# Performance work log

Hardware: AMD Instinct MI355X
Metric: run time of the kernel (lower is better)

The kernel has to match this reference:

```python
import jax, jax.numpy as jnp
import numpy as np


def setup_inputs() -> dict:
    key = jax.random.key(0)
    k1, k2, k3, k4 = jax.random.split(key, 4)
    B, S, E, H = 8, 2048, 1024, 64
    x = jax.random.normal(k1, (B, S, E), dtype=jnp.float32)
    # nn.Linear(E, H, bias=False) weight is (H, E); we store transposed (E, H)
    scale = 1.0 / np.sqrt(E)
    Wk = jax.random.normal(k2, (E, H), dtype=jnp.float32) * scale
    Wq = jax.random.normal(k3, (E, H), dtype=jnp.float32) * scale
    Wv = jax.random.normal(k4, (E, H), dtype=jnp.float32) * scale
    return {"x": x, "Wk": Wk, "Wq": Wq, "Wv": Wv}


def reference(x, Wk, Wq, Wv):
    # x: (B, S, E); projections: (B, S, H)
    k = x @ Wk
    q = x @ Wq
    v = x @ Wv
    H = k.shape[-1]
    # scores: (B, S, S) with 1/sqrt(H) scaling as in the torch code
    scores = jnp.einsum("bqh,bkh->bqk", q, k) * (H ** -0.5)
    S = x.shape[1]
    causal = jnp.triu(jnp.full((S, S), -jnp.inf, dtype=scores.dtype), k=1)
    wei = jax.nn.softmax(scores + causal, axis=-1)
    # dropout p=0.0 -> identity
    return jnp.einsum("bqk,bkh->bqh", wei, v)
```

## Files before the change

kernel.cpp:

```cpp
#include <hip/hip_runtime.h>
#include <hip/hip_bf16.h>

typedef unsigned short ushort_t;
typedef __attribute__((ext_vector_type(8))) short short8;
typedef __attribute__((ext_vector_type(4))) short short4v;
typedef __attribute__((ext_vector_type(4))) float f32x4;

__device__ __forceinline__ float bf2f(ushort_t u) {
    unsigned int x = ((unsigned int)u) << 16;
    float f; __builtin_memcpy(&f, &x, 4); return f;
}
__device__ __forceinline__ ushort_t f2bf(float f) {
    __hip_bfloat16 h = __float2bfloat16(f);
    ushort_t u; __builtin_memcpy(&u, &h, 2); return u;
}
__device__ __forceinline__ unsigned packbf2(float a, float b) {
    return (unsigned)f2bf(a) | ((unsigned)f2bf(b) << 16);
}

constexpr int E  = 1024;
constexpr int Hd = 64;
constexpr int S  = 2048;
constexpr int ROWS = 8 * 2048;
constexpr int NTOT = 192;
constexpr int LST  = 88;

__global__ __launch_bounds__(256)
void prep_wt(const float* __restrict__ Wk, const float* __restrict__ Wq,
             const float* __restrict__ Wv, ushort_t* __restrict__ WT)
{
    int idx = blockIdx.x * 256 + threadIdx.x;
    int n = idx >> 10;
    int kk = idx & 1023;
    const float* W = (n < 64) ? Wq : ((n < 128) ? Wk : Wv);
    int h = n & 63;
    WT[idx] = f2bf(W[kk * Hd + h]);
}

__global__ __launch_bounds__(256)
void proj_v7(const float* __restrict__ x, const ushort_t* __restrict__ WT,
             ushort_t* __restrict__ qo, ushort_t* __restrict__ ko,
             ushort_t* __restrict__ vTo)
{
    __shared__ alignas(16) ushort_t XS[32][LST];

    const int t    = threadIdx.x;
    const int w    = t >> 6;
    const int lane = t & 63;
    const int m    = lane & 15;
    const int g    = lane >> 4;
    const int rb   = blockIdx.x * 32;

    f32x4 accq[2], acck[2], accv[2];
    #pragma unroll
    for (int j = 0; j < 2; ++j) {
        accq[j] = (f32x4){0.f, 0.f, 0.f, 0.f};
        acck[j] = (f32x4){0.f, 0.f, 0.f, 0.f};
        accv[j] = (f32x4){0.f, 0.f, 0.f, 0.f};
    }

    const float* xptr = x + (size_t)(rb + (t >> 3)) * E + (t & 7) * 8;
    const ushort_t* wqp = WT + (size_t)(w * 16 + m) * E + g * 8;
    const ushort_t* wkp = wqp + (size_t)64 * E;
    const ushort_t* wvp = wqp + (size_t)128 * E;

    float4 xp0, xp1;
    short8 pbq[2], pbk[2], pbv[2], cbq[2], cbk[2], cbv[2];

    xp0 = *(const float4*)xptr;
    xp1 = *(const float4*)(xptr + 4);
    #pragma unroll
    for (int kt = 0; kt < 2; ++kt) {
        pbq[kt] = *(const short8*)(wqp + kt * 32);
        pbk[kt] = *(const short8*)(wkp + kt * 32);
        pbv[kt] = *(const short8*)(wvp + kt * 32);
    }

    #pragma unroll 1
    for (int c = 0; c < 16; ++c) {
        {
            uint4 sv;
            sv.x = packbf2(xp0.x, xp0.y);
            sv.y = packbf2(xp0.z, xp0.w);
            sv.z = packbf2(xp1.x, xp1.y);
            sv.w = packbf2(xp1.z, xp1.w);
            *(uint4*)&XS[t >> 3][(t & 7) * 8] = sv;
        }
        #pragma unroll
        for (int kt = 0; kt < 2; ++kt) {
            cbq[kt] = pbq[kt]; cbk[kt] = pbk[kt]; cbv[kt] = pbv[kt];
        }
        __syncthreads();

        if (c < 15) {
            const int k0 = (c + 1) * 64;
            xp0 = *(const float4*)(xptr + k0);
            xp1 = *(const float4*)(xptr + k0 + 4);
            #pragma unroll
            for (int kt = 0; kt < 2; ++kt) {
                pbq[kt] = *(const short8*)(wqp + k0 + kt * 32);
                pbk[kt] = *(const short8*)(wkp + k0 + kt * 32);
                pbv[kt] = *(const short8*)(wvp + k0 + kt * 32);
            }
        }

        #pragma unroll
        for (int kt = 0; kt < 2; ++kt) {
            short8 a0 = *(const short8*)&XS[m][kt * 32 + g * 8];
            short8 a1 = *(const short8*)&XS[16 + m][kt * 32 + g * 8];
            accq[0] = __builtin_amdgcn_mfma_f32_16x16x32_bf16(a0, cbq[kt], accq[0], 0, 0, 0);
            accq[1] = __builtin_amdgcn_mfma_f32_16x16x32_bf16(a1, cbq[kt], accq[1], 0, 0, 0);
            acck[0] = __builtin_amdgcn_mfma_f32_16x16x32_bf16(a0, cbk[kt], acck[0], 0, 0, 0);
            acck[1] = __builtin_amdgcn_mfma_f32_16x16x32_bf16(a1, cbk[kt], acck[1], 0, 0, 0);
            accv[0] = __builtin_amdgcn_mfma_f32_16x16x32_bf16(cbv[kt], a0, accv[0], 0, 0, 0);
            accv[1] = __builtin_amdgcn_mfma_f32_16x16x32_bf16(cbv[kt], a1, accv[1], 0, 0, 0);
        }
        __syncthreads();
    }

    const int col   = w * 16 + m;
    const int batch = rb >> 11;
    const int seq0  = rb & (S - 1);
    #pragma unroll
    for (int mt = 0; mt < 2; ++mt) {
        const int orow = rb + mt * 16 + g * 4;
        #pragma unroll
        for (int r = 0; r < 4; ++r) {
            qo[(size_t)(orow + r) * Hd + col] = f2bf(accq[mt][r] * 0.125f);
            ko[(size_t)(orow + r) * Hd + col] = f2bf(acck[mt][r]);
        }
    }
    #pragma unroll
    for (int ns = 0; ns < 2; ++ns)
        #pragma unroll
        for (int r = 0; r < 4; ++r) {
            const int h = w * 16 + g * 4 + r;
            vTo[(size_t)batch * Hd * S + (size_t)h * S + seq0 + ns * 16 + m]
                = f2bf(accv[ns][r]);
        }
}

__global__ __launch_bounds__(256)
void attn_part(const ushort_t* __restrict__ q, const ushort_t* __restrict__ k,
               const ushort_t* __restrict__ vT,
               float* __restrict__ lp, ushort_t* __restrict__ op)
{
    const int bi     = blockIdx.x;
    const int parity = bi & 3;
    const int pr     = bi >> 2;
    const int batch  = pr & 7;
    const int tile   = 31 - (pr >> 3);
    const int qs0    = tile * 64;
    const int sidx   = (batch * 32 + tile) * 4 + parity;

    const ushort_t* kb  = k  + (size_t)batch * S * Hd;
    const ushort_t* vTb = vT + (size_t)batch * Hd * S;

    const int t    = threadIdx.x;
    const int w    = t >> 6;
    const int lane = t & 63;
    const int m    = lane & 15;
    const int g    = lane >> 4;

    __shared__ alignas(16) ushort_t KS [64][LST];
    __shared__ alignas(16) ushort_t VTS[64][LST];

    const ushort_t* qrow = q + (size_t)(batch * S + qs0 + w * 16 + m) * Hd;
    short8 qf0 = *(const short8*)(qrow + g * 8);
    short8 qf1 = *(const short8*)(qrow + 32 + g * 8);

    f32x4 o[4];
    #pragma unroll
    for (int j = 0; j < 4; ++j) o[j] = (f32x4){0.f, 0.f, 0.f, 0.f};
    float lrun = 0.f;
    const int qr = w * 16 + m;

    const int r1 = t >> 3, c16 = (t & 7) * 8;
    uint4 pk0, pk1, pv0, pv1;

    int c = parity;
    if (c <= tile) {
        const int key0 = c * 64;
        const ushort_t* kt_base = kb + (size_t)key0 * Hd;
        pk0 = *(const uint4*)(kt_base + t * 8);
        pk1 = *(const uint4*)(kt_base + (t + 256) * 8);
        pv0 = *(const uint4*)(vTb + (size_t)r1 * S + key0 + c16);
        pv1 = *(const uint4*)(vTb + (size_t)(r1 + 32) * S + key0 + c16);
    }

    for (; c <= tile; c += 4) {
        *(uint4*)&KS [r1][c16]       = pk0;
        *(uint4*)&KS [r1 + 32][c16]  = pk1;
        *(uint4*)&VTS[r1][c16]       = pv0;
        *(uint4*)&VTS[r1 + 32][c16]  = pv1;
        __syncthreads();

        if (c + 4 <= tile) {
            const int key0n = (c + 4) * 64;
            const ushort_t* kt_base = kb + (size_t)key0n * Hd;
            pk0 = *(const uint4*)(kt_base + t * 8);
            pk1 = *(const uint4*)(kt_base + (t + 256) * 8);
            pv0 = *(const uint4*)(vTb + (size_t)r1 * S + key0n + c16);
            pv1 = *(const uint4*)(vTb + (size_t)(r1 + 32) * S + key0n + c16);
        }

        f32x4 sacc[4];
        #pragma unroll
        for (int j = 0; j < 4; ++j) sacc[j] = (f32x4){0.f, 0.f, 0.f, 0.f};
        #pragma unroll
        for (int nt = 0; nt < 4; ++nt) {
            short8 b0 = *(const short8*)&KS[nt * 16 + m][g * 8];
            short8 b1 = *(const short8*)&KS[nt * 16 + m][32 + g * 8];
            sacc[nt] = __builtin_amdgcn_mfma_f32_16x16x32_bf16(b0, qf0, sacc[nt], 0, 0, 0);
            sacc[nt] = __builtin_amdgcn_mfma_f32_16x16x32_bf16(b1, qf1, sacc[nt], 0, 0, 0);
        }

        if (c == tile) {
            #pragma unroll
            for (int nt = 0; nt < 4; ++nt)
                #pragma unroll
                for (int r = 0; r < 4; ++r) {
                    const int keyl = nt * 16 + g * 4 + r;
                    sacc[nt][r] = (keyl > qr) ? 0.f : __expf(sacc[nt][r]);
                }
        } else {
            #pragma unroll
            for (int nt = 0; nt < 4; ++nt)
                #pragma unroll
                for (int r = 0; r < 4; ++r)
                    sacc[nt][r] = __expf(sacc[nt][r]);
        }

        #pragma unroll
        for (int nt = 0; nt < 4; ++nt)
            lrun += (sacc[nt][0] + sacc[nt][1]) + (sacc[nt][2] + sacc[nt][3]);

        unsigned pw0[4], pw1[4];
        #pragma unroll
        for (int s = 0; s < 4; ++s) {
            pw0[s] = packbf2(sacc[s][0], sacc[s][1]);
            pw1[s] = packbf2(sacc[s][2], sacc[s][3]);
        }

        #pragma unroll
        for (int s = 0; s < 4; ++s) {
            short4v pa;
            { unsigned u2[2] = {pw0[s], pw1[s]}; __builtin_memcpy(&pa, u2, 8); }
            #pragma unroll
            for (int nt = 0; nt < 4; ++nt) {
                short4v vb = *(const short4v*)&VTS[nt * 16 + m][s * 16 + g * 4];
                o[nt] = __builtin_amdgcn_mfma_f32_16x16x16bf16_1k(pa, vb, o[nt], 0, 0, 0);
            }
        }
        __syncthreads();
    }

    {
        float ts = lrun;
        ts += __shfl_xor(ts, 16, 64);
        ts += __shfl_xor(ts, 32, 64);
        if (lane < 16) lp[sidx * 64 + w * 16 + m] = ts;
    }
    #pragma unroll
    for (int nt = 0; nt < 4; ++nt)
        #pragma unroll
        for (int r = 0; r < 4; ++r)
            op[(size_t)sidx * 4096 + (w * 16 + g * 4 + r) * 64 + nt * 16 + m]
                = f2bf(o[nt][r]);
}

__global__ __launch_bounds__(256)
void attn_merge(const float* __restrict__ lp, const ushort_t* __restrict__ op,
                float* __restrict__ out)
{
    const int bq    = blockIdx.x;
    const int batch = bq >> 5;
    const int tile  = bq & 31;
    const int s0    = (batch * 32 + tile) * 4;

    const int t   = threadIdx.x;
    const int row = t >> 2;
    const int c16 = (t & 3) * 16;

    float l = 0.f;
    #pragma unroll
    for (int p = 0; p < 4; ++p) l += lp[(s0 + p) * 64 + row];
    const float inv = 1.f / l;

    float acc[16];
    #pragma unroll
    for (int j = 0; j < 16; ++j) acc[j] = 0.f;
    #pragma unroll
    for (int p = 0; p < 4; ++p) {
        short8 a0 = *(const short8*)(op + (size_t)(s0 + p) * 4096 + row * 64 + c16);
        short8 a1 = *(const short8*)(op + (size_t)(s0 + p) * 4096 + row * 64 + c16 + 8);
        #pragma unroll
        for (int j = 0; j < 8; ++j) {
            acc[j]     += bf2f((ushort_t)a0[j]);
            acc[j + 8] += bf2f((ushort_t)a1[j]);
        }
    }
    float* dst = out + (size_t)(batch * S + tile * 64 + row) * Hd + c16;
    #pragma unroll
    for (int j = 0; j < 16; ++j) dst[j] = acc[j] * inv;
}

extern "C" void kernel_launch(void* const* d_in, const int* in_sizes, int n_in,
                              void* d_out, int out_size, void* d_ws, size_t ws_size,
                              hipStream_t stream) {
    const float* x  = (const float*)d_in[0];
    const float* Wk = (const float*)d_in[1];
    const float* Wq = (const float*)d_in[2];
    const float* Wv = (const float*)d_in[3];
    float* out = (float*)d_out;

    ushort_t* qws  = (ushort_t*)d_ws;
    ushort_t* kws  = qws + (size_t)ROWS * Hd;
    ushort_t* vTws = kws + (size_t)ROWS * Hd;
    ushort_t* WT   = vTws + (size_t)ROWS * Hd;
    float*    lpp  = (float*)(WT + (size_t)NTOT * E);
    ushort_t* opp  = (ushort_t*)(lpp + 1024 * 64);

    prep_wt<<<(NTOT * E) / 256, 256, 0, stream>>>(Wk, Wq, Wv, WT);
    proj_v7<<<ROWS / 32, 256, 0, stream>>>(x, WT, qws, kws, vTws);
    attn_part<<<1024, 256, 0, stream>>>(qws, kws, vTws, lpp, opp);
    attn_merge<<<256, 256, 0, stream>>>(lpp, opp, out);
}
```

Measured before the change: 133.5 us.

## Double-buffer LDS tiles in projection and attention to halve barriers

The projection kernel now alternates between two LDS buffers (XS0/XS1) with the K loop unrolled by two. This drops the trailing barrier per chunk, and the weight fragments for the next chunk are loaded just in time. The attention kernel double-buffers its K and V^T tiles, switching to a narrower row stride of 72, and removes the end-of-iteration barrier. The aim is to cut synchronisation stalls and overlap LDS writes with compute, at the cost of more LDS, which may lower occupancy. The narrower stride may also change bank-conflict behaviour.

```diff
diff --git a/kernel.cpp b/kernel.cpp
--- a/kernel.cpp
+++ b/kernel.cpp
@@ -24,6 +24,7 @@
 constexpr int ROWS = 8 * 2048;
 constexpr int NTOT = 192;
 constexpr int LST  = 88;
+constexpr int LSTA = 72;
 
 __global__ __launch_bounds__(256)
 void prep_wt(const float* __restrict__ Wk, const float* __restrict__ Wq,
@@ -42,7 +43,8 @@
              ushort_t* __restrict__ qo, ushort_t* __restrict__ ko,
              ushort_t* __restrict__ vTo)
 {
-    __shared__ alignas(16) ushort_t XS[32][LST];
+    __shared__ alignas(16) ushort_t XS0[32][LST];
+    __shared__ alignas(16) ushort_t XS1[32][LST];
 
     const int t    = threadIdx.x;
     const int w    = t >> 6;
@@ -64,58 +66,92 @@
     const ushort_t* wkp = wqp + (size_t)64 * E;
     const ushort_t* wvp = wqp + (size_t)128 * E;
 
-    float4 xp0, xp1;
-    short8 pbq[2], pbk[2], pbv[2], cbq[2], cbk[2], cbv[2];
-
-    xp0 = *(const float4*)xptr;
-    xp1 = *(const float4*)(xptr + 4);
+    const int sr = t >> 3, sc = (t & 7) * 8;
+
+    float4 xA0 = *(const float4*)xptr;
+    float4 xA1 = *(const float4*)(xptr + 4);
+    float4 xB0 = *(const float4*)(xptr + 64);
+    float4 xB1 = *(const float4*)(xptr + 64 + 4);
+
+    short8 wAq[2], wAk[2], wAv[2], wBq[2], wBk[2], wBv[2];
     #pragma unroll
     for (int kt = 0; kt < 2; ++kt) {
-        pbq[kt] = *(const short8*)(wqp + kt * 32);
-        pbk[kt] = *(const short8*)(wkp + kt * 32);
-        pbv[kt] = *(const short8*)(wvp + kt * 32);
+        wAq[kt] = *(const short8*)(wqp + kt * 32);
+        wAk[kt] = *(const short8*)(wkp + kt * 32);
+        wAv[kt] = *(const short8*)(wvp + kt * 32);
     }
 
     #pragma unroll 1
-    for (int c = 0; c < 16; ++c) {
+    for (int cc = 0; cc < 16; cc += 2) {
         {
             uint4 sv;
-            sv.x = packbf2(xp0.x, xp0.y);
-            sv.y = packbf2(xp0.z, xp0.w);
-            sv.z = packbf2(xp1.x, xp1.y);
-            sv.w = packbf2(xp1.z, xp1.w);
-            *(uint4*)&XS[t >> 3][(t & 7) * 8] = sv;
+            sv.x = packbf2(xA0.x, xA0.y);
+            sv.y = packbf2(xA0.z, xA0.w);
+            sv.z = packbf2(xA1.x, xA1.y);
+            sv.w = packbf2(xA1.z, xA1.w);
+            *(uint4*)&XS0[sr][sc] = sv;
+        }
+        __syncthreads();
+        if (cc + 2 < 16) {
+            const int k0 = (cc + 2) * 64;
+            xA0 = *(const float4*)(xptr + k0);
+            xA1 = *(const float4*)(xptr + k0 + 4);
+        }
+        {
+            const int k0 = (cc + 1) * 64;
+            #pragma unroll
+            for (int kt = 0; kt < 2; ++kt) {
+                wBq[kt] = *(const short8*)(wqp + k0 + kt * 32);
+                wBk[kt] = *(const short8*)(wkp + k0 + kt * 32);
+                wBv[kt] = *(const short8*)(wvp + k0 + kt * 32);
+            }
         }
         #pragma unroll
         for (int kt = 0; kt < 2; ++kt) {
-            cbq[kt] = pbq[kt]; cbk[kt] = pbk[kt]; cbv[kt] = pbv[kt];
+            short8 a0 = *(const short8*)&XS0[m][kt * 32 + g * 8];
+            short8 a1 = *(const short8*)&XS0[16 + m][kt * 32 + g * 8];
+            accq[0] = __builtin_amdgcn_mfma_f32_16x16x32_bf16(a0, wAq[kt], accq[0], 0, 0, 0);
+            accq[1] = __builtin_amdgcn_mfma_f32_16x16x32_bf16(a1, wAq[kt], accq[1], 0, 0, 0);
+            acck[0] = __builtin_amdgcn_mfma_f32_16x16x32_bf16(a0, wAk[kt], acck[0], 0, 0, 0);
+            acck[1] = __builtin_amdgcn_mfma_f32_16x16x32_bf16(a1, wAk[kt], acck[1], 0, 0, 0);
+            accv[0] = __builtin_amdgcn_mfma_f32_16x16x32_bf16(wAv[kt], a0, accv[0], 0, 0, 0);
+            accv[1] = __builtin_amdgcn_mfma_f32_16x16x32_bf16(wAv[kt], a1, accv[1], 0, 0, 0);
+        }
+
+        {
+            uint4 sv;
+            sv.x = packbf2(xB0.x, xB0.y);
+            sv.y = packbf2(xB0.z, xB0.w);
+            sv.z = packbf2(xB1.x, xB1.y);
+            sv.w = packbf2(xB1.z, xB1.w);
+            *(uint4*)&XS1[sr][sc] = sv;
         }
         __syncthreads();
-
-        if (c < 15) {
-            const int k0 = (c + 1) * 64;
-            xp0 = *(const float4*)(xptr + k0);
-            xp1 = *(const float4*)(xptr + k0 + 4);
+        if (cc + 3 < 16) {
+            const int k0 = (cc + 3) * 64;
+            xB0 = *(const float4*)(xptr + k0);
+            xB1 = *(const float4*)(xptr + k0 + 4);
+        }
+        if (cc + 2 < 16) {
+            const int k0 = (cc + 2) * 64;
             #pragma unroll
             for (int kt = 0; kt < 2; ++kt) {
-                pbq[kt] = *(const short8*)(wqp + k0 + kt * 32);
-                pbk[kt] = *(const short8*)(wkp + k0 + kt * 32);
-                pbv[kt] = *(const short8*)(wvp + k0 + kt * 32);
+                wAq[kt] = *(const short8*)(wqp + k0 + kt * 32);
+                wAk[kt] = *(const short8*)(wkp + k0 + kt * 32);
+                wAv[kt] = *(const short8*)(wvp + k0 + kt * 32);
             }
         }
-
         #pragma unroll
         for (int kt = 0; kt < 2; ++kt) {
-            short8 a0 = *(const short8*)&XS[m][kt * 32 + g * 8];
-            short8 a1 = *(const short8*)&XS[16 + m][kt * 32 + g * 8];
-            accq[0] = __builtin_amdgcn_mfma_f32_16x16x32_bf16(a0, cbq[kt], accq[0], 0, 0, 0);
-            accq[1] = __builtin_amdgcn_mfma_f32_16x16x32_bf16(a1, cbq[kt], accq[1], 0, 0, 0);
-            acck[0] = __builtin_amdgcn_mfma_f32_16x16x32_bf16(a0, cbk[kt], acck[0], 0, 0, 0);
-            acck[1] = __builtin_amdgcn_mfma_f32_16x16x32_bf16(a1, cbk[kt], acck[1], 0, 0, 0);
-            accv[0] = __builtin_amdgcn_mfma_f32_16x16x32_bf16(cbv[kt], a0, accv[0], 0, 0, 0);
-            accv[1] = __builtin_amdgcn_mfma_f32_16x16x32_bf16(cbv[kt], a1, accv[1], 0, 0, 0);
-        }
-        __syncthreads();
+            short8 a0 = *(const short8*)&XS1[m][kt * 32 + g * 8];
+            short8 a1 = *(const short8*)&XS1[16 + m][kt * 32 + g * 8];
+            accq[0] = __builtin_amdgcn_mfma_f32_16x16x32_bf16(a0, wBq[kt], accq[0], 0, 0, 0);
+            accq[1] = __builtin_amdgcn_mfma_f32_16x16x32_bf16(a1, wBq[kt], accq[1], 0, 0, 0);
+            acck[0] = __builtin_amdgcn_mfma_f32_16x16x32_bf16(a0, wBk[kt], acck[0], 0, 0, 0);
+            acck[1] = __builtin_amdgcn_mfma_f32_16x16x32_bf16(a1, wBk[kt], acck[1], 0, 0, 0);
+            accv[0] = __builtin_amdgcn_mfma_f32_16x16x32_bf16(wBv[kt], a0, accv[0], 0, 0, 0);
+            accv[1] = __builtin_amdgcn_mfma_f32_16x16x32_bf16(wBv[kt], a1, accv[1], 0, 0, 0);
+        }
     }
 
     const int col   = w * 16 + m;
@@ -162,8 +198,8 @@
     const int m    = lane & 15;
     const int g    = lane >> 4;
 
-    __shared__ alignas(16) ushort_t KS [64][LST];
-    __shared__ alignas(16) ushort_t VTS[64][LST];
+    __shared__ alignas(16) ushort_t KS [2][64][LSTA];
+    __shared__ alignas(16) ushort_t VTS[2][64][LSTA];
 
     const ushort_t* qrow = q + (size_t)(batch * S + qs0 + w * 16 + m) * Hd;
     short8 qf0 = *(const short8*)(qrow + g * 8);
@@ -188,11 +224,12 @@
         pv1 = *(const uint4*)(vTb + (size_t)(r1 + 32) * S + key0 + c16);
     }
 
-    for (; c <= tile; c += 4) {
-        *(uint4*)&KS [r1][c16]       = pk0;
-        *(uint4*)&KS [r1 + 32][c16]  = pk1;
-        *(uint4*)&VTS[r1][c16]       = pv0;
-        *(uint4*)&VTS[r1 + 32][c16]  = pv1;
+    int bit = 0;
+    for (; c <= tile; c += 4, bit ^= 1) {
+        *(uint4*)&KS [bit][r1][c16]       = pk0;
+        *(uint4*)&KS [bit][r1 + 32][c16]  = pk1;
+        *(uint4*)&VTS[bit][r1][c16]       = pv0;
+        *(uint4*)&VTS[bit][r1 + 32][c16]  = pv1;
         __syncthreads();
 
         if (c + 4 <= tile) {
@@ -209,8 +246,8 @@
         for (int j = 0; j < 4; ++j) sacc[j] = (f32x4){0.f, 0.f, 0.f, 0.f};
         #pragma unroll
         for (int nt = 0; nt < 4; ++nt) {
-            short8 b0 = *(const short8*)&KS[nt * 16 + m][g * 8];
-            short8 b1 = *(const short8*)&KS[nt * 16 + m][32 + g * 8];
+            short8 b0 = *(const short8*)&KS[bit][nt * 16 + m][g * 8];
+            short8 b1 = *(const short8*)&KS[bit][nt * 16 + m][32 + g * 8];
             sacc[nt] = __builtin_amdgcn_mfma_f32_16x16x32_bf16(b0, qf0, sacc[nt], 0, 0, 0);
             sacc[nt] = __builtin_amdgcn_mfma_f32_16x16x32_bf16(b1, qf1, sacc[nt], 0, 0, 0);
         }
@@ -248,11 +285,10 @@
             { unsigned u2[2] = {pw0[s], pw1[s]}; __builtin_memcpy(&pa, u2, 8); }
             #pragma unroll
             for (int nt = 0; nt < 4; ++nt) {
-                short4v vb = *(const short4v*)&VTS[nt * 16 + m][s * 16 + g * 4];
+                short4v vb = *(const short4v*)&VTS[bit][nt * 16 + m][s * 16 + g * 4];
                 o[nt] = __builtin_amdgcn_mfma_f32_16x16x16bf16_1k(pa, vb, o[nt], 0, 0, 0);
             }
         }
-        __syncthreads();
     }
 
     {
```

Measured after the change: 135.0 us. No clear change (+1.2%).

## Halve projection row tile and double-buffer x chunks with deeper prefetch

Applied to the files above, without the earlier changes.

The QKV projection kernel now handles 16 rows per block instead of 32, which doubles the grid to 1024 blocks for better occupancy and load balance. It alternates between two LDS buffers and keeps x prefetched four chunks ahead, with weights ping-ponged between two register sets, so global loads overlap MFMA work with one barrier per chunk instead of two. The trade-off is that each weight fragment now serves only one 16-row MFMA tile, which doubles total weight reads from L2, and vT stores become narrower.

```diff
diff --git a/kernel.cpp b/kernel.cpp
--- a/kernel.cpp
+++ b/kernel.cpp
@@ -23,7 +23,8 @@
 constexpr int S  = 2048;
 constexpr int ROWS = 8 * 2048;
 constexpr int NTOT = 192;
-constexpr int LST  = 88;
+constexpr int LSTP = 72;
+constexpr int LSTA = 88;
 
 __global__ __launch_bounds__(256)
 void prep_wt(const float* __restrict__ Wk, const float* __restrict__ Wq,
@@ -38,106 +39,161 @@
 }
 
 __global__ __launch_bounds__(256)
-void proj_v7(const float* __restrict__ x, const ushort_t* __restrict__ WT,
-             ushort_t* __restrict__ qo, ushort_t* __restrict__ ko,
-             ushort_t* __restrict__ vTo)
+void proj_v10(const float* __restrict__ x, const ushort_t* __restrict__ WT,
+              ushort_t* __restrict__ qo, ushort_t* __restrict__ ko,
+              ushort_t* __restrict__ vTo)
 {
-    __shared__ alignas(16) ushort_t XS[32][LST];
+    __shared__ alignas(16) ushort_t XS0[16][LSTP];
+    __shared__ alignas(16) ushort_t XS1[16][LSTP];
 
     const int t    = threadIdx.x;
     const int w    = t >> 6;
     const int lane = t & 63;
     const int m    = lane & 15;
     const int g    = lane >> 4;
-    const int rb   = blockIdx.x * 32;
-
-    f32x4 accq[2], acck[2], accv[2];
-    #pragma unroll
-    for (int j = 0; j < 2; ++j) {
-        accq[j] = (f32x4){0.f, 0.f, 0.f, 0.f};
-        acck[j] = (f32x4){0.f, 0.f, 0.f, 0.f};
-        accv[j] = (f32x4){0.f, 0.f, 0.f, 0.f};
-    }
-
-    const float* xptr = x + (size_t)(rb + (t >> 3)) * E + (t & 7) * 8;
+    const int rb   = blockIdx.x * 16;
+
+    f32x4 accq = (f32x4){0.f, 0.f, 0.f, 0.f};
+    f32x4 acck = (f32x4){0.f, 0.f, 0.f, 0.f};
+    f32x4 accv = (f32x4){0.f, 0.f, 0.f, 0.f};
+
+    const float* xptr = x + (size_t)(rb + (t >> 4)) * E + (t & 15) * 4;
     const ushort_t* wqp = WT + (size_t)(w * 16 + m) * E + g * 8;
     const ushort_t* wkp = wqp + (size_t)64 * E;
     const ushort_t* wvp = wqp + (size_t)128 * E;
 
-    float4 xp0, xp1;
-    short8 pbq[2], pbk[2], pbv[2], cbq[2], cbk[2], cbv[2];
-
-    xp0 = *(const float4*)xptr;
-    xp1 = *(const float4*)(xptr + 4);
+    const int sr = t >> 4, sc = (t & 15) * 4;
+
+    float4 xP0 = *(const float4*)(xptr);
+    float4 xP1 = *(const float4*)(xptr + 64);
+    float4 xP2 = *(const float4*)(xptr + 128);
+    float4 xP3 = *(const float4*)(xptr + 192);
+
+    short8 wAq[2], wAk[2], wAv[2], wBq[2], wBk[2], wBv[2];
     #pragma unroll
     for (int kt = 0; kt < 2; ++kt) {
-        pbq[kt] = *(const short8*)(wqp + kt * 32);
-        pbk[kt] = *(const short8*)(wkp + kt * 32);
-        pbv[kt] = *(const short8*)(wvp + kt * 32);
+        wAq[kt] = *(const short8*)(wqp + kt * 32);
+        wAk[kt] = *(const short8*)(wkp + kt * 32);
+        wAv[kt] = *(const short8*)(wvp + kt * 32);
     }
 
     #pragma unroll 1
-    for (int c = 0; c < 16; ++c) {
-        {
-            uint4 sv;
-            sv.x = packbf2(xp0.x, xp0.y);
-            sv.y = packbf2(xp0.z, xp0.w);
-            sv.z = packbf2(xp1.x, xp1.y);
-            sv.w = packbf2(xp1.z, xp1.w);
-            *(uint4*)&XS[t >> 3][(t & 7) * 8] = sv;
+    for (int cc = 0; cc < 16; cc += 4) {
+        {
+            uint2 sv;
+            sv.x = packbf2(xP0.x, xP0.y);
+            sv.y = packbf2(xP0.z, xP0.w);
+            *(uint2*)&XS0[sr][sc] = sv;
+        }
+        __syncthreads();
+        if (cc + 4 < 16) xP0 = *(const float4*)(xptr + (cc + 4) * 64);
+        {
+            const int k0 = (cc + 1) * 64;
+            #pragma unroll
+            for (int kt = 0; kt < 2; ++kt) {
+                wBq[kt] = *(const short8*)(wqp + k0 + kt * 32);
+                wBk[kt] = *(const short8*)(wkp + k0 + kt * 32);
+                wBv[kt] = *(const short8*)(wvp + k0 + kt * 32);
+            }
         }
         #pragma unroll
         for (int kt = 0; kt < 2; ++kt) {
-            cbq[kt] = pbq[kt]; cbk[kt] = pbk[kt]; cbv[kt] = pbv[kt];
-        }
-        __syncthreads();
-
-        if (c < 15) {
-            const int k0 = (c + 1) * 64;
-            xp0 = *(const float4*)(xptr + k0);
-            xp1 = *(const float4*)(xptr + k0 + 4);
+            short8 a0 = *(const short8*)&XS0[m][kt * 32 + g * 8];
+            accq = __builtin_amdgcn_mfma_f32_16x16x32_bf16(a0, wAq[kt], accq, 0, 0, 0);
+            acck = __builtin_amdgcn_mfma_f32_16x16x32_bf16(a0, wAk[kt], acck, 0, 0, 0);
+            accv = __builtin_amdgcn_mfma_f32_16x16x32_bf16(wAv[kt], a0, accv, 0, 0, 0);
+        }
+
+        {
+            uint2 sv;
+            sv.x = packbf2(xP1.x, xP1.y);
+            sv.y = packbf2(xP1.z, xP1.w);
+            *(uint2*)&XS1[sr][sc] = sv;
+        }
+        __syncthreads();
+        if (cc + 5 < 16) xP1 = *(const float4*)(xptr + (cc + 5) * 64);
+        if (cc + 2 < 16) {
+            const int k0 = (cc + 2) * 64;
             #pragma unroll
             for (int kt = 0; kt < 2; ++kt) {
-                pbq[kt] = *(const short8*)(wqp + k0 + kt * 32);
-                pbk[kt] = *(const short8*)(wkp + k0 + kt * 32);
-                pbv[kt] = *(const short8*)(wvp + k0 + kt * 32);
-            }
-        }
-
+                wAq[kt] = *(const short8*)(wqp + k0 + kt * 32);
+                wAk[kt] = *(const short8*)(wkp + k0 + kt * 32);
+                wAv[kt] = *(const short8*)(wvp + k0 + kt * 32);
+            }
+        }
         #pragma unroll
         for (int kt = 0; kt < 2; ++kt) {
-            short8 a0 = *(const short8*)&XS[m][kt * 32 + g * 8];
-            short8 a1 = *(const short8*)&XS[16 + m][kt * 32 + g * 8];
-            accq[0] = __builtin_amdgcn_mfma_f32_16x16x32_bf16(a0, cbq[kt], accq[0], 0, 0, 0);
-            accq[1] = __builtin_amdgcn_mfma_f32_16x16x32_bf16(a1, cbq[kt], accq[1], 0, 0, 0);
-            acck[0] = __builtin_amdgcn_mfma_f32_16x16x32_bf16(a0, cbk[kt], acck[0], 0, 0, 0);
-            acck[1] = __builtin_amdgcn_mfma_f32_16x16x32_bf16(a1, cbk[kt], acck[1], 0, 0, 0);
-            accv[0] = __builtin_amdgcn_mfma_f32_16x16x32_bf16(cbv[kt], a0, accv[0], 0, 0, 0);
-            accv[1] = __builtin_amdgcn_mfma_f32_16x16x32_bf16(cbv[kt], a1, accv[1], 0, 0, 0);
-        }
-        __syncthreads();
+            short8 a0 = *(const short8*)&XS1[m][kt * 32 + g * 8];
+            accq = __builtin_amdgcn_mfma_f32_16x16x32_bf16(a0, wBq[kt], accq, 0, 0, 0);
+            acck = __builtin_amdgcn_mfma_f32_16x16x32_bf16(a0, wBk[kt], acck, 0, 0, 0);
+            accv = __builtin_amdgcn_mfma_f32_16x16x32_bf16(wBv[kt], a0, accv, 0, 0, 0);
+        }
+
+        {
+            uint2 sv;
+            sv.x = packbf2(xP2.x, xP2.y);
+            sv.y = packbf2(xP2.z, xP2.w);
+            *(uint2*)&XS0[sr][sc] = sv;
+        }
+        __syncthreads();
+        if (cc + 6 < 16) xP2 = *(const float4*)(xptr + (cc + 6) * 64);
+        if (cc + 3 < 16) {
+            const int k0 = (cc + 3) * 64;
+            #pragma unroll
+            for (int kt = 0; kt < 2; ++kt) {
+                wBq[kt] = *(const short8*)(wqp + k0 + kt * 32);
+                wBk[kt] = *(const short8*)(wkp + k0 + kt * 32);
+                wBv[kt] = *(const short8*)(wvp + k0 + kt * 32);
+            }
+        }
+        #pragma unroll
+        for (int kt = 0; kt < 2; ++kt) {
+            short8 a0 = *(const short8*)&XS0[m][kt * 32 + g * 8];
+            accq = __builtin_amdgcn_mfma_f32_16x16x32_bf16(a0, wAq[kt], accq, 0, 0, 0);
+            acck = __builtin_amdgcn_mfma_f32_16x16x32_bf16(a0, wAk[kt], acck, 0, 0, 0);
+            accv = __builtin_amdgcn_mfma_f32_16x16x32_bf16(wAv[kt], a0, accv, 0, 0, 0);
+        }
+
+        {
+            uint2 sv;
+            sv.x = packbf2(xP3.x, xP3.y);
+            sv.y = packbf2(xP3.z, xP3.w);
+            *(uint2*)&XS1[sr][sc] = sv;
+        }
+        __syncthreads();
+        if (cc + 7 < 16) xP3 = *(const float4*)(xptr + (cc + 7) * 64);
+        if (cc + 4 < 16) {
+            const int k0 = (cc + 4) * 64;
+            #pragma unroll
+            for (int kt = 0; kt < 2; ++kt) {
+                wAq[kt] = *(const short8*)(wqp + k0 + kt * 32);
+                wAk[kt] = *(const short8*)(wkp + k0 + kt * 32);
+                wAv[kt] = *(const short8*)(wvp + k0 + kt * 32);
+            }
+        }
+        #pragma unroll
+        for (int kt = 0; kt < 2; ++kt) {
+            short8 a0 = *(const short8*)&XS1[m][kt * 32 + g * 8];
+            accq = __builtin_amdgcn_mfma_f32_16x16x32_bf16(a0, wBq[kt], accq, 0, 0, 0);
+            acck = __builtin_amdgcn_mfma_f32_16x16x32_bf16(a0, wBk[kt], acck, 0, 0, 0);
+            accv = __builtin_amdgcn_mfma_f32_16x16x32_bf16(wBv[kt], a0, accv, 0, 0, 0);
+        }
     }
 
     const int col   = w * 16 + m;
     const int batch = rb >> 11;
     const int seq0  = rb & (S - 1);
-    #pragma unroll
-    for (int mt = 0; mt < 2; ++mt) {
-        const int orow = rb + mt * 16 + g * 4;
-        #pragma unroll
-        for (int r = 0; r < 4; ++r) {
-            qo[(size_t)(orow + r) * Hd + col] = f2bf(accq[mt][r] * 0.125f);
-            ko[(size_t)(orow + r) * Hd + col] = f2bf(acck[mt][r]);
-        }
-    }
-    #pragma unroll
-    for (int ns = 0; ns < 2; ++ns)
-        #pragma unroll
-        for (int r = 0; r < 4; ++r) {
-            const int h = w * 16 + g * 4 + r;
-            vTo[(size_t)batch * Hd * S + (size_t)h * S + seq0 + ns * 16 + m]
-                = f2bf(accv[ns][r]);
-        }
+    const int orow  = rb + g * 4;
+    #pragma unroll
+    for (int r = 0; r < 4; ++r) {
+        qo[(size_t)(orow + r) * Hd + col] = f2bf(accq[r] * 0.125f);
+        ko[(size_t)(orow + r) * Hd + col] = f2bf(acck[r]);
+    }
+    #pragma unroll
+    for (int r = 0; r < 4; ++r) {
+        const int h = w * 16 + g * 4 + r;
+        vTo[(size_t)batch * Hd * S + (size_t)h * S + seq0 + m] = f2bf(accv[r]);
+    }
 }
 
 __global__ __launch_bounds__(256)
@@ -162,8 +218,8 @@
     const int m    = lane & 15;
     const int g    = lane >> 4;
 
-    __shared__ alignas(16) ushort_t KS [64][LST];
-    __shared__ alignas(16) ushort_t VTS[64][LST];
+    __shared__ alignas(16) ushort_t KS [64][LSTA];
+    __shared__ alignas(16) ushort_t VTS[64][LSTA];
 
     const ushort_t* qrow = q + (size_t)(batch * S + qs0 + w * 16 + m) * Hd;
     short8 qf0 = *(const short8*)(qrow + g * 8);
@@ -322,7 +378,7 @@
     ushort_t* opp  = (ushort_t*)(lpp + 1024 * 64);
 
     prep_wt<<<(NTOT * E) / 256, 256, 0, stream>>>(Wk, Wq, Wv, WT);
-    proj_v7<<<ROWS / 32, 256, 0, stream>>>(x, WT, qws, kws, vTws);
+    proj_v10<<<ROWS / 16, 256, 0, stream>>>(x, WT, qws, kws, vTws);
     attn_part<<<1024, 256, 0, stream>>>(qws, kws, vTws, lpp, opp);
     attn_merge<<<256, 256, 0, stream>>>(lpp, opp, out);
 }
```

Result: slower. 153.6 us (+15.1%).

## Double-buffer projection inputs via direct global-to-LDS loads with XOR swizzle

Applied to the files above, without the earlier changes.

Rewrites the QKV projection kernel so x (fp32) and the bf16 weight tiles are copied straight into LDS with global_load_lds, double-buffered so the next k-chunk streams in while the current one is computed. The bf16 conversion of x moves from the staging step to fragment read time, and XOR swizzled LDS layouts replace padding to avoid bank conflicts. Weights are now shared through LDS instead of each wave loading them into registers. This costs more LDS (fp32 x tile plus the full weight tile, doubled) and sets a two-blocks-per-SM launch bound, which may limit occupancy.

```diff
diff --git a/kernel.cpp b/kernel.cpp
--- a/kernel.cpp
+++ b/kernel.cpp
@@ -16,6 +16,12 @@
 }
 __device__ __forceinline__ unsigned packbf2(float a, float b) {
     return (unsigned)f2bf(a) | ((unsigned)f2bf(b) << 16);
+}
+
+__device__ __forceinline__ void gload16(const void* g, void* l) {
+    __builtin_amdgcn_global_load_lds(
+        (const __attribute__((address_space(1))) unsigned int*)g,
+        (__attribute__((address_space(3))) unsigned int*)l, 16, 0, 0);
 }
 
 constexpr int E  = 1024;
@@ -23,7 +29,7 @@
 constexpr int S  = 2048;
 constexpr int ROWS = 8 * 2048;
 constexpr int NTOT = 192;
-constexpr int LST  = 88;
+constexpr int LSTA = 88;
 
 __global__ __launch_bounds__(256)
 void prep_wt(const float* __restrict__ Wk, const float* __restrict__ Wq,
@@ -37,18 +43,20 @@
     WT[idx] = f2bf(W[kk * Hd + h]);
 }
 
-__global__ __launch_bounds__(256)
-void proj_v7(const float* __restrict__ x, const ushort_t* __restrict__ WT,
-             ushort_t* __restrict__ qo, ushort_t* __restrict__ ko,
-             ushort_t* __restrict__ vTo)
+__global__ __launch_bounds__(256, 2)
+void proj_v11(const float* __restrict__ x, const ushort_t* __restrict__ WT,
+              ushort_t* __restrict__ qo, ushort_t* __restrict__ ko,
+              ushort_t* __restrict__ vTo)
 {
-    __shared__ alignas(16) ushort_t XS[32][LST];
+    __shared__ alignas(16) float    XS[2][32 * 64];
+    __shared__ alignas(16) ushort_t WS[2][192 * 64];
 
     const int t    = threadIdx.x;
     const int w    = t >> 6;
     const int lane = t & 63;
     const int m    = lane & 15;
     const int g    = lane >> 4;
+    const int rl   = m & 7;
     const int rb   = blockIdx.x * 32;
 
     f32x4 accq[2], acck[2], accv[2];
@@ -59,62 +67,88 @@
         accv[j] = (f32x4){0.f, 0.f, 0.f, 0.f};
     }
 
-    const float* xptr = x + (size_t)(rb + (t >> 3)) * E + (t & 7) * 8;
-    const ushort_t* wqp = WT + (size_t)(w * 16 + m) * E + g * 8;
-    const ushort_t* wkp = wqp + (size_t)64 * E;
-    const ushort_t* wvp = wqp + (size_t)128 * E;
-
-    float4 xp0, xp1;
-    short8 pbq[2], pbk[2], pbv[2], cbq[2], cbk[2], cbv[2];
-
-    xp0 = *(const float4*)xptr;
-    xp1 = *(const float4*)(xptr + 4);
+    const int xrow0 = t >> 4;
+    const int xrow1 = (256 + t) >> 4;
+    const int xU0   = (t & 15) ^ (xrow0 & 7);
+    const int xU1   = (t & 15) ^ (xrow1 & 7);
+    const float* xs0 = x + (size_t)(rb + xrow0) * E + xU0 * 4;
+    const float* xs1 = x + (size_t)(rb + xrow1) * E + xU1 * 4;
+
+    const ushort_t* wsrc[6];
+    #pragma unroll
+    for (int j = 0; j < 6; ++j) {
+        const int L    = j * 256 + t;
+        const int wrow = L >> 3;
+        const int wU   = (L & 7) ^ (wrow & 7);
+        wsrc[j] = WT + (size_t)wrow * E + wU * 8;
+    }
+
+    int xiA[2][2], xiB[2][2];
+    #pragma unroll
+    for (int h = 0; h < 2; ++h)
+        #pragma unroll
+        for (int kt = 0; kt < 2; ++kt) {
+            const int row = h * 16 + m;
+            const int U   = kt * 8 + 2 * g;
+            xiA[h][kt] = (row * 16 + (U ^ rl)) * 4;
+            xiB[h][kt] = (row * 16 + ((U + 1) ^ rl)) * 4;
+        }
+    int wiq[2], wik[2], wiv[2];
     #pragma unroll
     for (int kt = 0; kt < 2; ++kt) {
-        pbq[kt] = *(const short8*)(wqp + kt * 32);
-        pbk[kt] = *(const short8*)(wkp + kt * 32);
-        pbv[kt] = *(const short8*)(wvp + kt * 32);
-    }
+        const int U = kt * 4 + g;
+        wiq[kt] = ((      w * 16 + m) * 8 + (U ^ rl)) * 8;
+        wik[kt] = ((64  + w * 16 + m) * 8 + (U ^ rl)) * 8;
+        wiv[kt] = ((128 + w * 16 + m) * 8 + (U ^ rl)) * 8;
+    }
+
+    auto STAGE = [&](int buf, int c) {
+        const int k0 = c * 64;
+        char* xb = (char*)&XS[buf][0];
+        char* wb = (char*)&WS[buf][0];
+        gload16(xs0 + k0, xb + (size_t)t * 16);
+        gload16(xs1 + k0, xb + (size_t)(256 + t) * 16);
+        #pragma unroll
+        for (int j = 0; j < 6; ++j)
+            gload16(wsrc[j] + k0, wb + (size_t)(j * 256 + t) * 16);
+    };
+
+    auto COMPUTE = [&](int buf) {
+        #pragma unroll
+        for (int kt = 0; kt < 2; ++kt) {
+            short8 fq = *(const short8*)&WS[buf][wiq[kt]];
+            short8 fk = *(const short8*)&WS[buf][wik[kt]];
+            short8 fv = *(const short8*)&WS[buf][wiv[kt]];
+            #pragma unroll
+            for (int h = 0; h < 2; ++h) {
+                float4 A = *(const float4*)&XS[buf][xiA[h][kt]];
+                float4 B = *(const float4*)&XS[buf][xiB[h][kt]];
+                short8 a;
+                {
+                    unsigned u4[4];
+                    u4[0] = packbf2(A.x, A.y);
+                    u4[1] = packbf2(A.z, A.w);
+                    u4[2] = packbf2(B.x, B.y);
+                    u4[3] = packbf2(B.z, B.w);
+                    __builtin_memcpy(&a, u4, 16);
+                }
+                accq[h] = __builtin_amdgcn_mfma_f32_16x16x32_bf16(a, fq, accq[h], 0, 0, 0);
+                acck[h] = __builtin_amdgcn_mfma_f32_16x16x32_bf16(a, fk, acck[h], 0, 0, 0);
+                accv[h] = __builtin_amdgcn_mfma_f32_16x16x32_bf16(fv, a, accv[h], 0, 0, 0);
+            }
+        }
+    };
+
+    STAGE(0, 0);
+    __syncthreads();
 
     #pragma unroll 1
-    for (int c = 0; c < 16; ++c) {
-        {
-            uint4 sv;
-            sv.x = packbf2(xp0.x, xp0.y);
-            sv.y = packbf2(xp0.z, xp0.w);
-            sv.z = packbf2(xp1.x, xp1.y);
-            sv.w = packbf2(xp1.z, xp1.w);
-            *(uint4*)&XS[t >> 3][(t & 7) * 8] = sv;
-        }
-        #pragma unroll
-        for (int kt = 0; kt < 2; ++kt) {
-            cbq[kt] = pbq[kt]; cbk[kt] = pbk[kt]; cbv[kt] = pbv[kt];
-        }
+    for (int cc = 0; cc < 16; cc += 2) {
+        STAGE(1, cc + 1);
+        COMPUTE(0);
         __syncthreads();
-
-        if (c < 15) {
-            const int k0 = (c + 1) * 64;
-            xp0 = *(const float4*)(xptr + k0);
-            xp1 = *(const float4*)(xptr + k0 + 4);
-            #pragma unroll
-            for (int kt = 0; kt < 2; ++kt) {
-                pbq[kt] = *(const short8*)(wqp + k0 + kt * 32);
-                pbk[kt] = *(const short8*)(wkp + k0 + kt * 32);
-                pbv[kt] = *(const short8*)(wvp + k0 + kt * 32);
-            }
-        }
-
-        #pragma unroll
-        for (int kt = 0; kt < 2; ++kt) {
-            short8 a0 = *(const short8*)&XS[m][kt * 32 + g * 8];
-            short8 a1 = *(const short8*)&XS[16 + m][kt * 32 + g * 8];
-            accq[0] = __builtin_amdgcn_mfma_f32_16x16x32_bf16(a0, cbq[kt], accq[0], 0, 0, 0);
-            accq[1] = __builtin_amdgcn_mfma_f32_16x16x32_bf16(a1, cbq[kt], accq[1], 0, 0, 0);
-            acck[0] = __builtin_amdgcn_mfma_f32_16x16x32_bf16(a0, cbk[kt], acck[0], 0, 0, 0);
-            acck[1] = __builtin_amdgcn_mfma_f32_16x16x32_bf16(a1, cbk[kt], acck[1], 0, 0, 0);
-            accv[0] = __builtin_amdgcn_mfma_f32_16x16x32_bf16(cbv[kt], a0, accv[0], 0, 0, 0);
-            accv[1] = __builtin_amdgcn_mfma_f32_16x16x32_bf16(cbv[kt], a1, accv[1], 0, 0, 0);
-        }
+        if (cc + 2 < 16) STAGE(0, cc + 2);
+        COMPUTE(1);
         __syncthreads();
     }
 
@@ -162,8 +196,8 @@
     const int m    = lane & 15;
     const int g    = lane >> 4;
 
-    __shared__ alignas(16) ushort_t KS [64][LST];
-    __shared__ alignas(16) ushort_t VTS[64][LST];
+    __shared__ alignas(16) ushort_t KS [64][LSTA];
+    __shared__ alignas(16) ushort_t VTS[64][LSTA];
 
     const ushort_t* qrow = q + (size_t)(batch * S + qs0 + w * 16 + m) * Hd;
     short8 qf0 = *(const short8*)(qrow + g * 8);
@@ -322,7 +356,7 @@
     ushort_t* opp  = (ushort_t*)(lpp + 1024 * 64);
 
     prep_wt<<<(NTOT * E) / 256, 256, 0, stream>>>(Wk, Wq, Wv, WT);
-    proj_v7<<<ROWS / 32, 256, 0, stream>>>(x, WT, qws, kws, vTws);
+    proj_v11<<<ROWS / 32, 256, 0, stream>>>(x, WT, qws, kws, vTws);
     attn_part<<<1024, 256, 0, stream>>>(qws, kws, vTws, lpp, opp);
     attn_merge<<<256, 256, 0, stream>>>(lpp, opp, out);
 }
```

Result: no change. 132.3 us (-0.8%).
